# Optimization experiments

Measured on AMD Instinct MI355X. Metric: run time of the kernel, lower is better.

The kernel has to match this reference:

```python
import jax, jax.numpy as jnp
import numpy as np

NUM_CLASSES = 100000   # vocab (input_dim of the layer)
DIM = 256              # embedding dim (output_dim of the layer)
BATCH = 256
NUM_TRUE = 1024        # hardcoded num_true in call()
NUM_SAMPLED = 16384    # hardcoded num_sampled in call()
LOG_RANGE = float(np.log(NUM_CLASSES + 1.0))


def _sample_log_uniform_unique(rng, n, range_max):
    # Mimics tf log_uniform_candidate_sampler with unique=True: rejection-sample
    # from P(c) ~ log((c+2)/(c+1)) until n unique ids are collected.
    seen = {}
    log_range = np.log(range_max + 1.0)
    while len(seen) < n:
        u = rng.uniform(0.0, log_range, size=2 * n)
        ids = np.minimum(np.floor(np.exp(u) - 1.0).astype(np.int64), range_max - 1)
        for v in ids.tolist():
            if len(seen) >= n:
                break
            seen[v] = None
    return np.fromiter(seen.keys(), dtype=np.int64, count=n)


def setup_inputs() -> dict:
    key = jax.random.key(0)
    k1, k2, k3, k4 = jax.random.split(key, 4)
    inputs = jax.random.normal(k1, (BATCH, DIM), jnp.float32)
    # Original inits w/b to zeros; use small random values for a non-degenerate baseline.
    w = jax.random.normal(k2, (NUM_CLASSES, DIM), jnp.float32) * 0.02
    b = jax.random.normal(k3, (NUM_CLASSES,), jnp.float32) * 0.02
    labels = jax.random.randint(k4, (BATCH, NUM_TRUE), 0, NUM_CLASSES, dtype=jnp.int32)
    rng = np.random.default_rng(0)
    sampled = jnp.asarray(_sample_log_uniform_unique(rng, NUM_SAMPLED, NUM_CLASSES), jnp.int32)
    return {"inputs": inputs, "w": w, "b": b, "labels": labels, "sampled": sampled}


def _log_uniform_prob(ids):
    idf = ids.astype(jnp.float32)
    return jnp.log((idf + 2.0) / (idf + 1.0)) / LOG_RANGE


def _expected_count(ids):
    # P(id appears among NUM_SAMPLED unique candidates) = 1 - (1-p)^NUM_SAMPLED
    p = _log_uniform_prob(ids)
    return -jnp.expm1(NUM_SAMPLED * jnp.log1p(-p))


def _sigmoid_xent(logits, target):
    # numerically stable sigmoid cross-entropy, target is a scalar label value
    return jnp.maximum(logits, 0.0) - logits * target + jnp.log1p(jnp.exp(-jnp.abs(logits)))


def reference(inputs, w, b, labels, sampled):
    # true logits: per-example dot with each true class row  [B, T]
    true_w = w[labels]                                    # [B, T, D] gather
    true_logits = jnp.einsum('bd,btd->bt', inputs, true_w) + b[labels]
    true_logits = true_logits - jnp.log(_expected_count(labels))
    # sampled logits: shared candidate set  [B, S]
    sampled_logits = inputs @ w[sampled].T + b[sampled]
    sampled_logits = sampled_logits - jnp.log(_expected_count(sampled))
    # NCE targets: 1/num_true for true classes, 0 for sampled; sum over columns
    true_xent = _sigmoid_xent(true_logits, 1.0 / NUM_TRUE)
    sampled_xent = _sigmoid_xent(sampled_logits, 0.0)
    return true_xent.sum(axis=1) + sampled_xent.sum(axis=1)   # [B]
```

## Files before the change

### kernel.cpp

```cpp
#include <hip/hip_runtime.h>
#include <hip/hip_bf16.h>

#define NUM_CLASSES 100000
#define DIM 256
#define BATCH 256
#define NUM_TRUE 1024
#define NUM_SAMPLED 16384
#define LOG_RANGE 11.51293546492023f
#define INV_LOG_RANGE (1.0f / LOG_RANGE)

#define SBLOCKS 512
#define TBLOCKS 2048

typedef __bf16 bf16x8 __attribute__((ext_vector_type(8)));
typedef float  f32x4  __attribute__((ext_vector_type(4)));

static __device__ __forceinline__ unsigned short f2bf(float f) {
    unsigned int u = __float_as_uint(f);
    unsigned int lsb = (u >> 16) & 1u;
    u += 0x7fffu + lsb;
    return (unsigned short)(u >> 16);
}

static __device__ __forceinline__ float neg_log_ec(int id) {
    float idf = (float)id;
    float p = logf((idf + 2.0f) / (idf + 1.0f)) * INV_LOG_RANGE;
    float ec = -expm1f((float)NUM_SAMPLED * log1pf(-p));
    return -logf(ec);
}

static __device__ __forceinline__ float dot4(float4 a, float4 b) {
    return fmaf(a.x, b.x, fmaf(a.y, b.y, fmaf(a.z, b.z, a.w * b.w)));
}

__global__ __launch_bounds__(256) void comb_kernel(const float* __restrict__ bias,
                                                   const float* __restrict__ inputs,
                                                   float* __restrict__ comb,
                                                   unsigned short* __restrict__ inbf) {
    int c = blockIdx.x * 256 + threadIdx.x;
    if (c < NUM_CLASSES) comb[c] = bias[c] + neg_log_ec(c);
    if (c < BATCH * DIM) inbf[c] = f2bf(inputs[c]);
}

__global__ __launch_bounds__(256) void fused_kernel(const float* __restrict__ inputs,
                                                    const float* __restrict__ w,
                                                    const float* __restrict__ comb,
                                                    const int* __restrict__ labels,
                                                    const int* __restrict__ sampled,
                                                    const unsigned short* __restrict__ inbf,
                                                    float* __restrict__ truep,
                                                    float* __restrict__ partial) {
    __shared__ unsigned short lw[32][264];
    __shared__ float cs[32];
    __shared__ float bacc[BATCH];
    __shared__ __align__(16) float ins[DIM];
    __shared__ float wsum[4];

    const int tid = threadIdx.x;

    if (blockIdx.x < SBLOCKS) {
        const int sblk = blockIdx.x;
        const int s0 = sblk * 32;
        bacc[tid] = 0.0f;

        const int inner = tid & 15;
        const int r16   = tid >> 4;
        #pragma unroll
        for (int rb = 0; rb < 2; ++rb) {
            const int r = rb * 16 + r16;
            const int id = sampled[s0 + r];
            const float* src = w + (size_t)id * DIM;
            #pragma unroll
            for (int j = 0; j < 4; ++j) {
                float4 v = *(const float4*)(src + j * 64 + inner * 4);
                ushort4 pk;
                pk.x = f2bf(v.x); pk.y = f2bf(v.y); pk.z = f2bf(v.z); pk.w = f2bf(v.w);
                *(ushort4*)(&lw[r][j * 64 + inner * 4]) = pk;
            }
        }
        if (tid < 32) cs[tid] = comb[sampled[s0 + tid]];
        __syncthreads();

        const int lane = tid & 63;
        const int wv   = tid >> 6;
        const int m    = lane & 15;
        const int quad = lane >> 4;
        const int shalf = (wv >> 1) * 16;
        const int bhalf = (wv & 1) * 128;

        bf16x8 af[8];
        #pragma unroll
        for (int kk = 0; kk < 8; ++kk)
            af[kk] = *(const bf16x8*)(&lw[shalf + m][kk * 32 + quad * 8]);

        #pragma unroll
        for (int t = 0; t < 8; ++t) {
            const int brow = bhalf + t * 16 + m;
            const unsigned short* bp = inbf + brow * DIM;
            bf16x8 bf[8];
            #pragma unroll
            for (int kk = 0; kk < 8; ++kk)
                bf[kk] = *(const bf16x8*)(bp + kk * 32 + quad * 8);
            f32x4 acc = {0, 0, 0, 0};
            #pragma unroll
            for (int kk = 0; kk < 8; ++kk)
                acc = __builtin_amdgcn_mfma_f32_16x16x32_bf16(af[kk], bf[kk], acc, 0, 0, 0);
            float ps = 0.0f;
            #pragma unroll
            for (int r = 0; r < 4; ++r) {
                float c = cs[shalf + quad * 4 + r];
                float l = acc[r] + c;
                ps += fmaxf(l, 0.0f) + __logf(1.0f + __expf(-fabsf(l)));
            }
            ps += __shfl_xor(ps, 16); ps += __shfl_xor(ps, 32);
            if (quad == 0) atomicAdd(&bacc[bhalf + t * 16 + m], ps);
        }
        __syncthreads();
        partial[tid * SBLOCKS + sblk] = bacc[tid];
    } else {
        const int bid  = blockIdx.x - SBLOCKS;
        const int b    = bid >> 3;
        const int chnk = bid & 7;
        ins[tid] = inputs[b * DIM + tid];
        __syncthreads();

        const int lane = tid & 63;
        const int wv   = tid >> 6;
        const int sub  = lane >> 4;
        const int part = lane & 15;
        const float4* ir = (const float4*)ins;
        const float4 in0 = ir[part], in1 = ir[16 + part], in2 = ir[32 + part], in3 = ir[48 + part];

        const int* lab = labels + b * NUM_TRUE + chnk * 128 + wv * 32;

        float4 buf[2][4];
        float  cb[2];
        #pragma unroll
        for (int s = 0; s < 2; ++s) {
            int l = lab[s * 4 + sub];
            const float4* wr = (const float4*)(w + (size_t)l * DIM);
            buf[s][0] = wr[part];      buf[s][1] = wr[16 + part];
            buf[s][2] = wr[32 + part]; buf[s][3] = wr[48 + part];
            cb[s] = comb[l];
        }

        float acc = 0.0f;
        #pragma unroll
        for (int i = 0; i < 8; ++i) {
            const int cur = i & 1;
            float4 w0 = buf[cur][0], w1 = buf[cur][1], w2 = buf[cur][2], w3 = buf[cur][3];
            float cl = cb[cur];
            if (i < 6) {
                int l = lab[(i + 2) * 4 + sub];
                const float4* wr = (const float4*)(w + (size_t)l * DIM);
                buf[cur][0] = wr[part];      buf[cur][1] = wr[16 + part];
                buf[cur][2] = wr[32 + part]; buf[cur][3] = wr[48 + part];
                cb[cur] = comb[l];
            }
            float d = dot4(w0, in0) + dot4(w1, in1) + dot4(w2, in2) + dot4(w3, in3);
            d += __shfl_xor(d, 1); d += __shfl_xor(d, 2);
            d += __shfl_xor(d, 4); d += __shfl_xor(d, 8);
            float logit = d + cl;
            float v = fmaxf(logit, 0.0f) - logit * (1.0f / (float)NUM_TRUE)
                    + __logf(1.0f + __expf(-fabsf(logit)));
            acc += (part == 0) ? v : 0.0f;
        }
        acc += __shfl_xor(acc, 16); acc += __shfl_xor(acc, 32);
        if (lane == 0) wsum[wv] = acc;
        __syncthreads();
        if (tid == 0) truep[b * 8 + chnk] = wsum[0] + wsum[1] + wsum[2] + wsum[3];
    }
}

__global__ __launch_bounds__(256) void reduce_kernel(const float* __restrict__ partial,
                                                     const float* __restrict__ truep,
                                                     float* __restrict__ out) {
    __shared__ float wsum[4];
    const int b = blockIdx.x;
    const int tid = threadIdx.x;
    float v = partial[b * SBLOCKS + tid] + partial[b * SBLOCKS + 256 + tid];
    if (tid < 8) v += truep[b * 8 + tid];
    v += __shfl_xor(v, 1);  v += __shfl_xor(v, 2);  v += __shfl_xor(v, 4);
    v += __shfl_xor(v, 8);  v += __shfl_xor(v, 16); v += __shfl_xor(v, 32);
    if ((tid & 63) == 0) wsum[tid >> 6] = v;
    __syncthreads();
    if (tid == 0) out[b] = wsum[0] + wsum[1] + wsum[2] + wsum[3];
}

extern "C" void kernel_launch(void* const* d_in, const int* in_sizes, int n_in,
                              void* d_out, int out_size, void* d_ws, size_t ws_size,
                              hipStream_t stream) {
    const float* inputs  = (const float*)d_in[0];
    const float* w       = (const float*)d_in[1];
    const float* bias    = (const float*)d_in[2];
    const int*   labels  = (const int*)d_in[3];
    const int*   sampled = (const int*)d_in[4];
    float* out = (float*)d_out;

    float*          comb    = (float*)d_ws;
    unsigned short* inbf    = (unsigned short*)((char*)d_ws + 409600);
    float*          truep   = (float*)((char*)d_ws + 540672);
    float*          partial = (float*)((char*)d_ws + 548864);

    comb_kernel<<<(NUM_CLASSES + 255) / 256, 256, 0, stream>>>(bias, inputs, comb, inbf);
    fused_kernel<<<SBLOCKS + TBLOCKS, 256, 0, stream>>>(inputs, w, comb, labels,
                                                        sampled, inbf, truep, partial);
    reduce_kernel<<<BATCH, 256, 0, stream>>>(partial, truep, out);
}
```

Before: 178.7 us.

## Replace reduce kernel with global atomics and halve true-logit block count

Drops the separate reduce kernel and the partial/truep workspace buffers. The output is zeroed in comb_kernel, and the sampled and true blocks then atomically add their per-batch sums straight into out. The true-logit path now uses 1024 blocks, each covering 256 labels with a 16-step double-buffered loop instead of 8. The aim is to save a kernel launch and the partial-buffer round trip; the cost is 256 x 512 float atomics contending on 256 addresses, fewer blocks for latency hiding, and a summation order that is no longer deterministic.

```diff
diff --git a/kernel.cpp b/kernel.cpp
--- a/kernel.cpp
+++ b/kernel.cpp
@@ -10,7 +10,7 @@
 #define INV_LOG_RANGE (1.0f / LOG_RANGE)
 
 #define SBLOCKS 512
-#define TBLOCKS 2048
+#define TBLOCKS 1024
 
 typedef __bf16 bf16x8 __attribute__((ext_vector_type(8)));
 typedef float  f32x4  __attribute__((ext_vector_type(4)));
@@ -36,10 +36,12 @@
 __global__ __launch_bounds__(256) void comb_kernel(const float* __restrict__ bias,
                                                    const float* __restrict__ inputs,
                                                    float* __restrict__ comb,
-                                                   unsigned short* __restrict__ inbf) {
+                                                   unsigned short* __restrict__ inbf,
+                                                   float* __restrict__ out) {
     int c = blockIdx.x * 256 + threadIdx.x;
     if (c < NUM_CLASSES) comb[c] = bias[c] + neg_log_ec(c);
     if (c < BATCH * DIM) inbf[c] = f2bf(inputs[c]);
+    if (c < BATCH) out[c] = 0.0f;
 }
 
 __global__ __launch_bounds__(256) void fused_kernel(const float* __restrict__ inputs,
@@ -48,8 +50,7 @@
                                                     const int* __restrict__ labels,
                                                     const int* __restrict__ sampled,
                                                     const unsigned short* __restrict__ inbf,
-                                                    float* __restrict__ truep,
-                                                    float* __restrict__ partial) {
+                                                    float* __restrict__ out) {
     __shared__ unsigned short lw[32][264];
     __shared__ float cs[32];
     __shared__ float bacc[BATCH];
@@ -116,11 +117,11 @@
             if (quad == 0) atomicAdd(&bacc[bhalf + t * 16 + m], ps);
         }
         __syncthreads();
-        partial[tid * SBLOCKS + sblk] = bacc[tid];
+        atomicAdd(&out[tid], bacc[tid]);
     } else {
         const int bid  = blockIdx.x - SBLOCKS;
-        const int b    = bid >> 3;
-        const int chnk = bid & 7;
+        const int b    = bid >> 2;
+        const int chnk = bid & 3;
         ins[tid] = inputs[b * DIM + tid];
         __syncthreads();
 
@@ -131,7 +132,7 @@
         const float4* ir = (const float4*)ins;
         const float4 in0 = ir[part], in1 = ir[16 + part], in2 = ir[32 + part], in3 = ir[48 + part];
 
-        const int* lab = labels + b * NUM_TRUE + chnk * 128 + wv * 32;
+        const int* lab = labels + b * NUM_TRUE + chnk * 256 + wv * 64;
 
         float4 buf[2][4];
         float  cb[2];
@@ -146,11 +147,11 @@
 
         float acc = 0.0f;
         #pragma unroll
-        for (int i = 0; i < 8; ++i) {
+        for (int i = 0; i < 16; ++i) {
             const int cur = i & 1;
             float4 w0 = buf[cur][0], w1 = buf[cur][1], w2 = buf[cur][2], w3 = buf[cur][3];
             float cl = cb[cur];
-            if (i < 6) {
+            if (i < 14) {
                 int l = lab[(i + 2) * 4 + sub];
                 const float4* wr = (const float4*)(w + (size_t)l * DIM);
                 buf[cur][0] = wr[part];      buf[cur][1] = wr[16 + part];
@@ -168,23 +169,8 @@
         acc += __shfl_xor(acc, 16); acc += __shfl_xor(acc, 32);
         if (lane == 0) wsum[wv] = acc;
         __syncthreads();
-        if (tid == 0) truep[b * 8 + chnk] = wsum[0] + wsum[1] + wsum[2] + wsum[3];
+        if (tid == 0) atomicAdd(&out[b], wsum[0] + wsum[1] + wsum[2] + wsum[3]);
     }
-}
-
-__global__ __launch_bounds__(256) void reduce_kernel(const float* __restrict__ partial,
-                                                     const float* __restrict__ truep,
-                                                     float* __restrict__ out) {
-    __shared__ float wsum[4];
-    const int b = blockIdx.x;
-    const int tid = threadIdx.x;
-    float v = partial[b * SBLOCKS + tid] + partial[b * SBLOCKS + 256 + tid];
-    if (tid < 8) v += truep[b * 8 + tid];
-    v += __shfl_xor(v, 1);  v += __shfl_xor(v, 2);  v += __shfl_xor(v, 4);
-    v += __shfl_xor(v, 8);  v += __shfl_xor(v, 16); v += __shfl_xor(v, 32);
-    if ((tid & 63) == 0) wsum[tid >> 6] = v;
-    __syncthreads();
-    if (tid == 0) out[b] = wsum[0] + wsum[1] + wsum[2] + wsum[3];
 }
 
 extern "C" void kernel_launch(void* const* d_in, const int* in_sizes, int n_in,
@@ -197,13 +183,10 @@
     const int*   sampled = (const int*)d_in[4];
     float* out = (float*)d_out;
 
-    float*          comb    = (float*)d_ws;
-    unsigned short* inbf    = (unsigned short*)((char*)d_ws + 409600);
-    float*          truep   = (float*)((char*)d_ws + 540672);
-    float*          partial = (float*)((char*)d_ws + 548864);
+    float*          comb = (float*)d_ws;
+    unsigned short* inbf = (unsigned short*)((char*)d_ws + 409600);
 
-    comb_kernel<<<(NUM_CLASSES + 255) / 256, 256, 0, stream>>>(bias, inputs, comb, inbf);
+    comb_kernel<<<(NUM_CLASSES + 255) / 256, 256, 0, stream>>>(bias, inputs, comb, inbf, out);
     fused_kernel<<<SBLOCKS + TBLOCKS, 256, 0, stream>>>(inputs, w, comb, labels,
-                                                        sampled, inbf, truep, partial);
-    reduce_kernel<<<BATCH, 256, 0, stream>>>(partial, truep, out);
+                                                        sampled, inbf, out);
 }
```

Result: slower. 187.1 us (+4.7%).
